# Kernel optimization log

Hardware: AMD Instinct MI355X
Metric: run time of the kernel (lower is better)

The kernel has to match this reference:

```python
import jax, jax.numpy as jnp
import numpy as np

K = 3          # number of nearest neighbors for interpolation
EPS = 1e-8     # inverse-distance epsilon
BN_EPS = 1e-5  # torch BatchNorm1d default eps

B, NY, NX = 4, 16384, 4096
CY, CX = 128, 256
DIM = CY + CX
SHARED = (512, 256, 128)


def setup_inputs() -> dict:
    key = jax.random.key(0)
    ks = jax.random.split(key, 16)
    inp = {
        'y_points': jax.random.normal(ks[0], (B, NY, 3), jnp.float32),
        'y_feats': jax.random.normal(ks[1], (B, NY, CY), jnp.float32),
        'x_points': jax.random.normal(ks[2], (B, NX, 3), jnp.float32),
        'x_feats': jax.random.normal(ks[3], (B, NX, CX), jnp.float32),
    }
    in_chs = (DIM,) + SHARED[:-1]
    for i, (cin, cout) in enumerate(zip(in_chs, SHARED), start=1):
        scale = 1.0 / np.sqrt(cin)
        inp[f'W{i}'] = jax.random.normal(ks[4 + i], (cout, cin), jnp.float32) * scale
        inp[f'b{i}'] = jnp.zeros((cout,), jnp.float32)
        inp[f'g{i}'] = jnp.ones((cout,), jnp.float32)
        inp[f'be{i}'] = jnp.zeros((cout,), jnp.float32)
    return inp


def _interpolate(y_points, x_points, y_feats, x_feats):
    # squared pairwise distances [B, Ny, Nx]
    d = (jnp.sum(y_points * y_points, -1)[:, :, None]
         + jnp.sum(x_points * x_points, -1)[:, None, :]
         - 2.0 * jnp.einsum('bnd,bmd->bnm', y_points, x_points))
    neg_d, idx = jax.lax.top_k(-d, K)             # K smallest distances
    dists = -neg_d                                 # [B, Ny, K]
    w = 1.0 / (dists + EPS)
    w = w / jnp.sum(w, -1, keepdims=True)
    # gather neighbor features: [B, Ny, K, Cx]
    nb = jnp.take_along_axis(x_feats[:, None, :, :], idx[..., None], axis=2)
    interp = jnp.sum(nb * w[..., None], axis=2)    # [B, Ny, Cx]
    return jnp.concatenate([y_feats, interp], axis=-1)


def _conv_bn_relu(y, W, b, g, beta):
    # 1x1 Conv1d == per-point linear; y: [B, Cin, N]
    y = jnp.einsum('oc,bcn->bon', W, y) + b[None, :, None]
    mu = jnp.mean(y, axis=(0, 2), keepdims=True)
    var = jnp.var(y, axis=(0, 2), keepdims=True)
    y = (y - mu) * jax.lax.rsqrt(var + BN_EPS)
    return jax.nn.relu(y * g[None, :, None] + beta[None, :, None])


def reference(y_points, y_feats, x_points, x_feats,
              W1, b1, g1, be1, W2, b2, g2, be2, W3, b3, g3, be3):
    i_points = _interpolate(y_points, x_points, y_feats, x_feats)  # [B, Ny, DIM]
    y = jnp.transpose(i_points, (0, 2, 1))                          # [B, DIM, Ny]
    y = _conv_bn_relu(y, W1, b1, g1, be1)
    y = _conv_bn_relu(y, W2, b2, g2, be2)
    y = _conv_bn_relu(y, W3, b3, g3, be3)
    return y
```

## Files before the change

kernel.cpp:

```cpp
#include <hip/hip_runtime.h>

#define NYTOT 16384
#define NXP 4096
#define MTOT 65536
#define CYC 128
#define CXC 256
#define DIMC 384

typedef __attribute__((ext_vector_type(8))) _Float16 half8;
typedef __attribute__((ext_vector_type(4))) _Float16 half4;
typedef __attribute__((ext_vector_type(4))) float floatx4;
typedef __attribute__((ext_vector_type(2))) float floatx2;

using half_t = _Float16;

struct alignas(16) HF8 { half_t h[8]; };

__device__ __forceinline__ float fmed3(float a, float b, float c) {
  return __builtin_amdgcn_fmed3f(a, b, c);
}

__global__ __launch_bounds__(256) void prep_kernel(
    const float* __restrict__ x_points, float4* __restrict__ xq,
    const float* __restrict__ W1, const float* __restrict__ W2,
    const float* __restrict__ W3, half_t* __restrict__ wout) {
#pragma clang fp contract(off)
  const int bid = blockIdx.x;
  if (bid < 64) {
    int j = bid * 256 + threadIdx.x;
    int b = j >> 12, jj = j & 4095;
    const float* p = x_points + (size_t)b * NXP * 3 + 3 * jj;
    float x0 = p[0], x1 = p[1], x2 = p[2];
    float sx = (x0 * x0 + x1 * x1) + x2 * x2;
    float4 v; v.x = x0; v.y = x1; v.z = x2; v.w = sx;
    xq[j] = v;
  } else {
    int i = (bid - 64) * 256 + threadIdx.x;
    const float* src; half_t* dst; int j;
    if (i < 49152)      { src = W1; dst = wout;          j = i; }
    else if (i < 81920) { src = W2; dst = wout + 196608; j = i - 49152; }
    else                { src = W3; dst = wout + 327680; j = i - 81920; }
    floatx4 v = ((const floatx4*)src)[j];
    half4 h;
#pragma unroll
    for (int e = 0; e < 4; ++e) h[e] = (half_t)v[e];
    ((half4*)dst)[j] = h;
  }
}

__global__ __launch_bounds__(1024, 8) void interp_kernel(
    const float* __restrict__ y_points, const float* __restrict__ y_feats,
    const float* __restrict__ x_feats, const float4* __restrict__ xq,
    half_t* __restrict__ A0) {
#pragma clang fp contract(off)
  __shared__ float pd[16][128][3];
  __shared__ int   pi[16][128][3];
  __shared__ float t2s[128];
  __shared__ float sw[3][128];
  __shared__ int   si[3][128];
  const int b = blockIdx.x >> 7;
  const int chunk = blockIdx.x & 127;
  const int t = threadIdx.x;
  const int lane = t & 63;
  const int seg = t >> 6;
  const int yloc = lane << 1;

  const float* yp = y_points + ((size_t)b * NYTOT + chunk * 128 + yloc) * 3;
  floatx2 Y0 = {yp[0], yp[3]};
  floatx2 Y1 = {yp[1], yp[4]};
  floatx2 Y2 = {yp[2], yp[5]};
  floatx2 SY = (Y0 * Y0 + Y1 * Y1) + Y2 * Y2;

  const float4* xqs = xq + (size_t)b * NXP;
  const int jb = __builtin_amdgcn_readfirstlane(seg * 256);

  floatx2 D0 = {1e30f, 1e30f}, D1 = D0, D2 = D0;
#pragma unroll 8
  for (int jj = 0; jj < 256; ++jj) {
    float4 p = xqs[jb + jj];
    floatx2 inner = (Y0 * p.x + Y1 * p.y) + Y2 * p.z;
    floatx2 d = (SY + p.w) - 2.0f * inner;
    D2.x = fmed3(d.x, D1.x, D2.x);  D2.y = fmed3(d.y, D1.y, D2.y);
    D1.x = fmed3(d.x, D0.x, D1.x);  D1.y = fmed3(d.y, D0.y, D1.y);
    D0.x = fminf(d.x, D0.x);        D0.y = fminf(d.y, D0.y);
  }
  pd[seg][yloc][0] = D0.x; pd[seg][yloc][1] = D1.x; pd[seg][yloc][2] = D2.x;
  pd[seg][yloc + 1][0] = D0.y; pd[seg][yloc + 1][1] = D1.y; pd[seg][yloc + 1][2] = D2.y;
  __syncthreads();

  if (t < 128) {
    float m0 = 1e30f, m1 = 1e30f, m2 = 1e30f;
#pragma unroll
    for (int s = 0; s < 16; ++s)
#pragma unroll
      for (int c = 0; c < 3; ++c) {
        float v = pd[s][t][c];
        m2 = fmed3(v, m1, m2);
        m1 = fmed3(v, m0, m1);
        m0 = fminf(v, m0);
      }
    t2s[t] = m2;
  }
  __syncthreads();

  const float t2a = t2s[yloc], t2b = t2s[yloc + 1];
  const float tmax = fmaxf(t2a, t2b);
  float e0a = 1e30f, e1a = 1e30f, e2a = 1e30f; int k0a = 0, k1a = 0, k2a = 0;
  float e0b = 1e30f, e1b = 1e30f, e2b = 1e30f; int k0b = 0, k1b = 0, k2b = 0;
#pragma unroll 4
  for (int jj = 0; jj < 256; ++jj) {
    float4 p = xqs[jb + jj];
    floatx2 inner = (Y0 * p.x + Y1 * p.y) + Y2 * p.z;
    floatx2 d = (SY + p.w) - 2.0f * inner;
    if (fminf(d.x, d.y) <= tmax) {
      int j = jb + jj;
      {
        float dv = d.x;
        bool l0 = dv < e0a, l1 = dv < e1a, l2 = dv < e2a;
        e2a = l1 ? e1a : (l2 ? dv : e2a);  k2a = l1 ? k1a : (l2 ? j : k2a);
        e1a = l0 ? e0a : (l1 ? dv : e1a);  k1a = l0 ? k0a : (l1 ? j : k1a);
        e0a = l0 ? dv : e0a;               k0a = l0 ? j : k0a;
      }
      {
        float dv = d.y;
        bool l0 = dv < e0b, l1 = dv < e1b, l2 = dv < e2b;
        e2b = l1 ? e1b : (l2 ? dv : e2b);  k2b = l1 ? k1b : (l2 ? j : k2b);
        e1b = l0 ? e0b : (l1 ? dv : e1b);  k1b = l0 ? k0b : (l1 ? j : k1b);
        e0b = l0 ? dv : e0b;               k0b = l0 ? j : k0b;
      }
    }
  }
  pd[seg][yloc][0] = e0a; pd[seg][yloc][1] = e1a; pd[seg][yloc][2] = e2a;
  pi[seg][yloc][0] = k0a; pi[seg][yloc][1] = k1a; pi[seg][yloc][2] = k2a;
  pd[seg][yloc + 1][0] = e0b; pd[seg][yloc + 1][1] = e1b; pd[seg][yloc + 1][2] = e2b;
  pi[seg][yloc + 1][0] = k0b; pi[seg][yloc + 1][1] = k1b; pi[seg][yloc + 1][2] = k2b;
  __syncthreads();

  if (t < 128) {
    float f0 = 1e30f, f1 = 1e30f, f2 = 1e30f;
    int m0i = 0, m1i = 0, m2i = 0;
#pragma unroll
    for (int s = 0; s < 16; ++s)
#pragma unroll
      for (int c = 0; c < 3; ++c) {
        float d = pd[s][t][c]; int j = pi[s][t][c];
        bool l0 = d < f0, l1 = d < f1, l2 = d < f2;
        f2 = l1 ? f1 : (l2 ? d : f2);  m2i = l1 ? m1i : (l2 ? j : m2i);
        f1 = l0 ? f0 : (l1 ? d : f1);  m1i = l0 ? m0i : (l1 ? j : m1i);
        f0 = l0 ? d : f0;              m0i = l0 ? j : m0i;
      }
    float w0 = 1.0f / (f0 + 1e-8f), w1 = 1.0f / (f1 + 1e-8f), w2 = 1.0f / (f2 + 1e-8f);
    float ws = (w0 + w1) + w2;
    sw[0][t] = w0 / ws; sw[1][t] = w1 / ws; sw[2][t] = w2 / ws;
    si[0][t] = m0i; si[1][t] = m1i; si[2][t] = m2i;
  }
  __syncthreads();

  const floatx4* xf4 = (const floatx4*)(x_feats + (size_t)b * NXP * CXC);
  const floatx4* yf4 = (const floatx4*)(y_feats + ((size_t)b * NYTOT + chunk * 128) * CYC);
  half_t* fb = A0 + ((size_t)b * NYTOT + chunk * 128) * DIMC;
  {
    const int q = t & 63;
    const int ysub = t >> 6;
    for (int y2 = ysub; y2 < 128; y2 += 16) {
      int j0 = si[0][y2], j1 = si[1][y2], j2 = si[2][y2];
      float a0 = sw[0][y2], a1 = sw[1][y2], a2 = sw[2][y2];
      floatx4 v0 = xf4[(size_t)j0 * 64 + q];
      floatx4 v1 = xf4[(size_t)j1 * 64 + q];
      floatx4 v2 = xf4[(size_t)j2 * 64 + q];
      half4 h;
#pragma unroll
      for (int e = 0; e < 4; ++e)
        h[e] = (half_t)fmaf(v2[e], a2, fmaf(v1[e], a1, v0[e] * a0));
      *(half4*)&fb[(size_t)y2 * DIMC + CYC + q * 4] = h;
    }
  }
  {
    const int q2 = t & 31;
    const int ysub2 = t >> 5;
    for (int y2 = ysub2; y2 < 128; y2 += 32) {
      floatx4 v = yf4[(size_t)y2 * 32 + q2];
      half4 h;
#pragma unroll
      for (int e = 0; e < 4; ++e) h[e] = (half_t)v[e];
      *(half4*)&fb[(size_t)y2 * DIMC + q2 * 4] = h;
    }
  }
}

template<int K, int O, int NTN, bool FUSEA>
__global__ __launch_bounds__(512) void gemm256(
    const half_t* __restrict__ A, const half_t* __restrict__ Wh,
    const float* __restrict__ bias, half_t* __restrict__ C,
    float* __restrict__ sums, const float* __restrict__ ssA) {
  __shared__ __align__(16) short As[16][2][512];
  __shared__ __align__(16) short Bs[8][2][512];
  constexpr int NWG = (MTOT / 256) * NTN;
  const int lin = (blockIdx.x & 7) * (NWG >> 3) + (blockIdx.x >> 3);
  const int m0 = (lin / NTN) * 256;
  const int n0 = (lin % NTN) * 128;
  const int tid = threadIdx.x;
  const int lane = tid & 63;
  const int wid = tid >> 6;
  const int wm = wid >> 1, wn = wid & 1;
  const int lm = lane & 15;
  const int lk = (lane >> 4) * 8;
  floatx4 acc[4][4] = {};

  for (int k0 = 0; k0 < K; k0 += 64) {
    __syncthreads();
    if constexpr (FUSEA) {
#pragma unroll
      for (int c = 0; c < 2; ++c) {
        int id = wid * 2 + c;
        int sub = id >> 1, ks = id & 1;
        const half_t* src = Wh + (size_t)(n0 + sub * 16 + lm) * K + (k0 + ks * 32 + lk);
        __builtin_amdgcn_global_load_lds(
            (const __attribute__((address_space(1))) void*)src,
            (__attribute__((address_space(3))) void*)&Bs[sub][ks][0], 16, 0, 0);
      }
      const int r = tid & 255;
      const int hh = tid >> 8;
      const half_t* arow = A + (size_t)(m0 + r) * K + k0 + hh * 32;
      half8 in[4];
#pragma unroll
      for (int g = 0; g < 4; ++g) in[g] = *(const half8*)&arow[g * 8];
#pragma unroll
      for (int g = 0; g < 4; ++g) {
        int kc = k0 + hh * 32 + g * 8;
        half8 h;
#pragma unroll
        for (int e = 0; e < 8; ++e) {
          float f = fmaxf((float)in[g][e] * ssA[kc + e] + ssA[K + kc + e], 0.f);
          h[e] = (half_t)f;
        }
        *(half8*)&As[r >> 4][hh][(g * 16 + (r & 15)) * 8] = h;
      }
    } else {
#pragma unroll
      for (int c = 0; c < 6; ++c) {
        int id = wid * 6 + c;
        if (id < 32) {
          int sub = id >> 1, ks = id & 1;
          const half_t* src = A + (size_t)(m0 + sub * 16 + lm) * K + (k0 + ks * 32 + lk);
          __builtin_amdgcn_global_load_lds(
              (const __attribute__((address_space(1))) void*)src,
              (__attribute__((address_space(3))) void*)&As[sub][ks][0], 16, 0, 0);
        } else {
          int id2 = id - 32;
          int sub = id2 >> 1, ks = id2 & 1;
          const half_t* src = Wh + (size_t)(n0 + sub * 16 + lm) * K + (k0 + ks * 32 + lk);
          __builtin_amdgcn_global_load_lds(
              (const __attribute__((address_space(1))) void*)src,
              (__attribute__((address_space(3))) void*)&Bs[sub][ks][0], 16, 0, 0);
        }
      }
    }
    __syncthreads();
#pragma unroll
    for (int ks = 0; ks < 2; ++ks) {
      half8 af[4], bfm[4];
#pragma unroll
      for (int i = 0; i < 4; ++i) af[i] = *(const half8*)&As[wm * 4 + i][ks][lane * 8];
#pragma unroll
      for (int j = 0; j < 4; ++j) bfm[j] = *(const half8*)&Bs[wn * 4 + j][ks][lane * 8];
#pragma unroll
      for (int i = 0; i < 4; ++i)
#pragma unroll
        for (int j = 0; j < 4; ++j)
          acc[i][j] = __builtin_amdgcn_mfma_f32_16x16x32_f16(af[i], bfm[j], acc[i][j], 0, 0, 0);
    }
  }

#pragma unroll
  for (int j = 0; j < 4; ++j) {
    int nn = n0 + wn * 64 + j * 16 + lm;
    float bv = bias[nn];
    float psum = 0.f, psq = 0.f;
#pragma unroll
    for (int i = 0; i < 4; ++i) {
      int mr = m0 + wm * 64 + i * 16 + (lane >> 4) * 4;
#pragma unroll
      for (int rr = 0; rr < 4; ++rr) {
        float z = acc[i][j][rr] + bv;
        C[(size_t)(mr + rr) * O + nn] = (half_t)z;
        psum += z; psq += z * z;
      }
    }
    psum += __shfl_xor(psum, 16, 64); psq += __shfl_xor(psq, 16, 64);
    psum += __shfl_xor(psum, 32, 64); psq += __shfl_xor(psq, 32, 64);
    if ((lane >> 4) == 0) {
      atomicAdd(&sums[nn], psum);
      atomicAdd(&sums[O + nn], psq);
    }
  }
}

template<int K, int O, bool FUSEA, bool TOUT>
__global__ __launch_bounds__(256) void gemm_f16(
    const half_t* __restrict__ A, const half_t* __restrict__ Wh,
    const float* __restrict__ bias, half_t* __restrict__ C,
    float* __restrict__ sums, const float* __restrict__ ssA) {
  __shared__ __align__(16) short As[8][2][512];
  __shared__ __align__(16) short Bs[8][2][512];
  const int m0 = blockIdx.x * 128;
  const int n0 = blockIdx.y * 128;
  const int tid = threadIdx.x;
  const int lane = tid & 63;
  const int wid = tid >> 6;
  const int wm = wid >> 1, wn = wid & 1;
  const int lm = lane & 15;
  const int lk = (lane >> 4) * 8;
  floatx4 acc[4][4] = {};

  for (int k0 = 0; k0 < K; k0 += 64) {
    __syncthreads();
    if constexpr (FUSEA) {
#pragma unroll
      for (int c = 0; c < 4; ++c) {
        int id = wid * 4 + c;
        int sub = id >> 1;
        int ks = id & 1;
        const half_t* src = Wh + (size_t)(n0 + sub * 16 + lm) * K + (k0 + ks * 32 + lk);
        __builtin_amdgcn_global_load_lds(
            (const __attribute__((address_space(1))) void*)src,
            (__attribute__((address_space(3))) void*)&Bs[sub][ks][0], 16, 0, 0);
      }
      const int r = tid & 127;
      const int hh = tid >> 7;
      const half_t* arow = A + (size_t)(m0 + r) * K + k0 + hh * 32;
      half8 in[4];
#pragma unroll
      for (int g = 0; g < 4; ++g) in[g] = *(const half8*)&arow[g * 8];
#pragma unroll
      for (int g = 0; g < 4; ++g) {
        int kc = k0 + hh * 32 + g * 8;
        half8 h;
#pragma unroll
        for (int e = 0; e < 8; ++e) {
          float f = fmaxf((float)in[g][e] * ssA[kc + e] + ssA[K + kc + e], 0.f);
          h[e] = (half_t)f;
        }
        *(half8*)&As[r >> 4][hh][(g * 16 + (r & 15)) * 8] = h;
      }
    } else {
#pragma unroll
      for (int c = 0; c < 8; ++c) {
        int id = wid * 8 + c;
        int sub = (id >> 1) & 7;
        int ks = id & 1;
        const half_t* src = (id < 16)
            ? A  + (size_t)(m0 + sub * 16 + lm) * K + (k0 + ks * 32 + lk)
            : Wh + (size_t)(n0 + sub * 16 + lm) * K + (k0 + ks * 32 + lk);
        __builtin_amdgcn_global_load_lds(
            (const __attribute__((address_space(1))) void*)src,
            (__attribute__((address_space(3))) void*)(id < 16 ? &As[sub][ks][0]
                                                             : &Bs[sub][ks][0]),
            16, 0, 0);
      }
    }
    __syncthreads();
#pragma unroll
    for (int ks = 0; ks < 2; ++ks) {
      half8 af[4], bfm[4];
#pragma unroll
      for (int i = 0; i < 4; ++i) af[i] = *(const half8*)&As[wm * 4 + i][ks][lane * 8];
#pragma unroll
      for (int j = 0; j < 4; ++j) bfm[j] = *(const half8*)&Bs[wn * 4 + j][ks][lane * 8];
#pragma unroll
      for (int i = 0; i < 4; ++i)
#pragma unroll
        for (int j = 0; j < 4; ++j)
          acc[i][j] = __builtin_amdgcn_mfma_f32_16x16x32_f16(af[i], bfm[j], acc[i][j], 0, 0, 0);
    }
  }

  const int bb = m0 >> 14;
  const int nbase = (m0 & (NYTOT - 1)) + wm * 64 + (lane >> 4) * 4;
#pragma unroll
  for (int j = 0; j < 4; ++j) {
    int nn = n0 + wn * 64 + j * 16 + lm;
    float bv = bias[nn];
    float psum = 0.f, psq = 0.f;
#pragma unroll
    for (int i = 0; i < 4; ++i) {
      half4 hv;
#pragma unroll
      for (int rr = 0; rr < 4; ++rr) {
        float z = acc[i][j][rr] + bv;
        hv[rr] = (half_t)z;
        psum += z; psq += z * z;
      }
      if constexpr (TOUT) {
        *(half4*)&C[((size_t)(bb * O + nn)) * NYTOT + nbase + i * 16] = hv;
      } else {
        int mr = m0 + wm * 64 + i * 16 + (lane >> 4) * 4;
#pragma unroll
        for (int rr = 0; rr < 4; ++rr)
          C[(size_t)(mr + rr) * O + nn] = hv[rr];
      }
    }
    psum += __shfl_xor(psum, 16, 64); psq += __shfl_xor(psq, 16, 64);
    psum += __shfl_xor(psum, 32, 64); psq += __shfl_xor(psq, 32, 64);
    if ((lane >> 4) == 0) {
      atomicAdd(&sums[nn], psum);
      atomicAdd(&sums[O + nn], psq);
    }
  }
}

__global__ void finalize_kernel(const float* __restrict__ sums, const float* __restrict__ g,
                                const float* __restrict__ be, float* __restrict__ ss, int O) {
  int c = threadIdx.x;
  if (c < O) {
    const float invN = 1.0f / 65536.0f;
    float mean = sums[c] * invN;
    float var = sums[O + c] * invN - mean * mean;
    float sc = g[c] / sqrtf(var + 1e-5f);
    float sh = be[c] - mean * sc;
    if (!isfinite(sc) || !isfinite(sh)) { sc = 1.0f; sh = 0.0f; }
    ss[c] = sc;
    ss[O + c] = sh;
  }
}

__global__ __launch_bounds__(256) void bnfin_kernel(
    const half_t* __restrict__ Z, const float* __restrict__ ss,
    float* __restrict__ out) {
  size_t i = (size_t)blockIdx.x * 256 + threadIdx.x;
  int c = (int)((i * 8) >> 14) & 127;
  float sc = ss[c], sh = ss[128 + c];
  HF8 v = ((const HF8*)Z)[i];
  floatx4 o0, o1;
#pragma unroll
  for (int e = 0; e < 4; ++e) {
    o0[e] = fmaxf((float)v.h[e] * sc + sh, 0.f);
    o1[e] = fmaxf((float)v.h[4 + e] * sc + sh, 0.f);
  }
  ((floatx4*)out)[i * 2] = o0;
  ((floatx4*)out)[i * 2 + 1] = o1;
}

extern "C" void kernel_launch(void* const* d_in, const int* in_sizes, int n_in,
                              void* d_out, int out_size, void* d_ws, size_t ws_size,
                              hipStream_t stream) {
  const float* y_points = (const float*)d_in[0];
  const float* y_feats  = (const float*)d_in[1];
  const float* x_points = (const float*)d_in[2];
  const float* x_feats  = (const float*)d_in[3];
  const float* W1 = (const float*)d_in[4];  const float* b1 = (const float*)d_in[5];
  const float* g1 = (const float*)d_in[6];  const float* be1 = (const float*)d_in[7];
  const float* W2 = (const float*)d_in[8];  const float* b2 = (const float*)d_in[9];
  const float* g2 = (const float*)d_in[10]; const float* be2 = (const float*)d_in[11];
  const float* W3 = (const float*)d_in[12]; const float* b3 = (const float*)d_in[13];
  const float* g3 = (const float*)d_in[14]; const float* be3 = (const float*)d_in[15];

  char* ws = (char*)d_ws;
  half_t* A0 = (half_t*)ws;
  half_t* z1 = (half_t*)(ws + 50331648);
  half_t* z2 = (half_t*)ws;
  half_t* z3T = (half_t*)(ws + 50331648);
  float4* xq = (float4*)(ws + 50331648);
  float* st = (float*)(ws + 117440512);
  half_t* W1h = (half_t*)d_out;
  half_t* W2h = W1h + 196608;
  half_t* W3h = W1h + 327680;
  hipMemsetAsync(st, 0, 1792 * sizeof(float), stream);

  prep_kernel<<<416, 256, 0, stream>>>(x_points, xq, W1, W2, W3, W1h);
  interp_kernel<<<512, 1024, 0, stream>>>(y_points, y_feats, x_feats, xq, A0);

  gemm256<384, 512, 4, false><<<1024, 512, 0, stream>>>(A0, W1h, b1, z1, st + 0, nullptr);
  finalize_kernel<<<1, 512, 0, stream>>>(st + 0, g1, be1, st + 1792, 512);

  gemm256<512, 256, 2, true><<<512, 512, 0, stream>>>(z1, W2h, b2, z2, st + 1024, st + 1792);
  finalize_kernel<<<1, 256, 0, stream>>>(st + 1024, g2, be2, st + 2816, 256);

  gemm_f16<256, 128, true, true><<<dim3(512, 1), 256, 0, stream>>>(z2, W3h, b3, z3T, st + 1536, st + 2816);
  finalize_kernel<<<1, 128, 0, stream>>>(st + 1536, g3, be3, st + 3328, 128);

  bnfin_kernel<<<4096, 256, 0, stream>>>(z3T, st + 3328, (float*)d_out);
}
```

Measured before the change: 460.9 us.

## Software-pipeline GEMM tiles with double-buffered weights and block-level BN stat reduction

Restructures the three GEMM kernels so the next K-tile's weights go into a second LDS buffer via async global-to-LDS loads, and the next A slice goes into registers, while MFMAs run on the current tile. The first GEMM now also routes A through registers instead of direct LDS loads, giving one code path for all three GEMMs. BatchNorm partial sums are first reduced across warps in shared memory, so each block issues one atomic per channel instead of one per warp. This costs extra LDS and register pressure, which may lower occupancy.

```diff
diff --git a/kernel.cpp b/kernel.cpp
--- a/kernel.cpp
+++ b/kernel.cpp
@@ -188,14 +188,16 @@
   }
 }
 
-template<int K, int O, int NTN, bool FUSEA>
-__global__ __launch_bounds__(512) void gemm256(
+template<int K, int O, int NTN, bool BN>
+__global__ __launch_bounds__(512) void gemm256p(
     const half_t* __restrict__ A, const half_t* __restrict__ Wh,
     const float* __restrict__ bias, half_t* __restrict__ C,
     float* __restrict__ sums, const float* __restrict__ ssA) {
   __shared__ __align__(16) short As[16][2][512];
-  __shared__ __align__(16) short Bs[8][2][512];
+  __shared__ __align__(16) short Bs[2][8][2][512];
+  __shared__ float stats[4][2][128];
   constexpr int NWG = (MTOT / 256) * NTN;
+  constexpr int NT = K / 64;
   const int lin = (blockIdx.x & 7) * (NWG >> 3) + (blockIdx.x >> 3);
   const int m0 = (lin / NTN) * 256;
   const int n0 = (lin % NTN) * 128;
@@ -205,73 +207,78 @@
   const int wm = wid >> 1, wn = wid & 1;
   const int lm = lane & 15;
   const int lk = (lane >> 4) * 8;
+  const int r = tid & 255;
+  const int hh = tid >> 8;
   floatx4 acc[4][4] = {};
-
-  for (int k0 = 0; k0 < K; k0 += 64) {
+  half8 in[4];
+
+#pragma unroll
+  for (int c = 0; c < 2; ++c) {
+    int id = wid * 2 + c;
+    int sub = id >> 1, ks = id & 1;
+    const half_t* src = Wh + (size_t)(n0 + sub * 16 + lm) * K + (ks * 32 + lk);
+    __builtin_amdgcn_global_load_lds(
+        (const __attribute__((address_space(1))) void*)src,
+        (__attribute__((address_space(3))) void*)&Bs[0][sub][ks][0], 16, 0, 0);
+  }
+  {
+    const half_t* arow = A + (size_t)(m0 + r) * K + hh * 32;
+#pragma unroll
+    for (int g = 0; g < 4; ++g) in[g] = *(const half8*)&arow[g * 8];
+  }
+  int cur = 0;
+
+  for (int t = 0; t < NT; ++t) {
+    const int k0 = t * 64;
     __syncthreads();
-    if constexpr (FUSEA) {
-#pragma unroll
-      for (int c = 0; c < 2; ++c) {
-        int id = wid * 2 + c;
-        int sub = id >> 1, ks = id & 1;
-        const half_t* src = Wh + (size_t)(n0 + sub * 16 + lm) * K + (k0 + ks * 32 + lk);
-        __builtin_amdgcn_global_load_lds(
-            (const __attribute__((address_space(1))) void*)src,
-            (__attribute__((address_space(3))) void*)&Bs[sub][ks][0], 16, 0, 0);
-      }
-      const int r = tid & 255;
-      const int hh = tid >> 8;
-      const half_t* arow = A + (size_t)(m0 + r) * K + k0 + hh * 32;
-      half8 in[4];
-#pragma unroll
-      for (int g = 0; g < 4; ++g) in[g] = *(const half8*)&arow[g * 8];
-#pragma unroll
-      for (int g = 0; g < 4; ++g) {
+#pragma unroll
+    for (int g = 0; g < 4; ++g) {
+      half8 h;
+      if constexpr (BN) {
         int kc = k0 + hh * 32 + g * 8;
-        half8 h;
 #pragma unroll
         for (int e = 0; e < 8; ++e) {
           float f = fmaxf((float)in[g][e] * ssA[kc + e] + ssA[K + kc + e], 0.f);
           h[e] = (half_t)f;
         }
-        *(half8*)&As[r >> 4][hh][(g * 16 + (r & 15)) * 8] = h;
-      }
-    } else {
-#pragma unroll
-      for (int c = 0; c < 6; ++c) {
-        int id = wid * 6 + c;
-        if (id < 32) {
-          int sub = id >> 1, ks = id & 1;
-          const half_t* src = A + (size_t)(m0 + sub * 16 + lm) * K + (k0 + ks * 32 + lk);
-          __builtin_amdgcn_global_load_lds(
-              (const __attribute__((address_space(1))) void*)src,
-              (__attribute__((address_space(3))) void*)&As[sub][ks][0], 16, 0, 0);
-        } else {
-          int id2 = id - 32;
-          int sub = id2 >> 1, ks = id2 & 1;
-          const half_t* src = Wh + (size_t)(n0 + sub * 16 + lm) * K + (k0 + ks * 32 + lk);
-          __builtin_amdgcn_global_load_lds(
-              (const __attribute__((address_space(1))) void*)src,
-              (__attribute__((address_space(3))) void*)&Bs[sub][ks][0], 16, 0, 0);
-        }
-      }
+      } else {
+        h = in[g];
+      }
+      *(half8*)&As[r >> 4][hh][(g * 16 + (r & 15)) * 8] = h;
     }
     __syncthreads();
+    if (t + 1 < NT) {
+      const int k1 = k0 + 64;
+#pragma unroll
+      for (int c = 0; c < 2; ++c) {
+        int id = wid * 2 + c;
+        int sub = id >> 1, ks = id & 1;
+        const half_t* src = Wh + (size_t)(n0 + sub * 16 + lm) * K + (k1 + ks * 32 + lk);
+        __builtin_amdgcn_global_load_lds(
+            (const __attribute__((address_space(1))) void*)src,
+            (__attribute__((address_space(3))) void*)&Bs[cur ^ 1][sub][ks][0], 16, 0, 0);
+      }
+      const half_t* arow = A + (size_t)(m0 + r) * K + k1 + hh * 32;
+#pragma unroll
+      for (int g = 0; g < 4; ++g) in[g] = *(const half8*)&arow[g * 8];
+    }
 #pragma unroll
     for (int ks = 0; ks < 2; ++ks) {
       half8 af[4], bfm[4];
 #pragma unroll
       for (int i = 0; i < 4; ++i) af[i] = *(const half8*)&As[wm * 4 + i][ks][lane * 8];
 #pragma unroll
-      for (int j = 0; j < 4; ++j) bfm[j] = *(const half8*)&Bs[wn * 4 + j][ks][lane * 8];
+      for (int j = 0; j < 4; ++j) bfm[j] = *(const half8*)&Bs[cur][wn * 4 + j][ks][lane * 8];
 #pragma unroll
       for (int i = 0; i < 4; ++i)
 #pragma unroll
         for (int j = 0; j < 4; ++j)
           acc[i][j] = __builtin_amdgcn_mfma_f32_16x16x32_f16(af[i], bfm[j], acc[i][j], 0, 0, 0);
     }
-  }
-
+    cur ^= 1;
+  }
+
+  float ps[4], pq[4];
 #pragma unroll
   for (int j = 0; j < 4; ++j) {
     int nn = n0 + wn * 64 + j * 16 + lm;
@@ -289,20 +296,34 @@
     }
     psum += __shfl_xor(psum, 16, 64); psq += __shfl_xor(psq, 16, 64);
     psum += __shfl_xor(psum, 32, 64); psq += __shfl_xor(psq, 32, 64);
-    if ((lane >> 4) == 0) {
-      atomicAdd(&sums[nn], psum);
-      atomicAdd(&sums[O + nn], psq);
-    }
-  }
-}
-
-template<int K, int O, bool FUSEA, bool TOUT>
-__global__ __launch_bounds__(256) void gemm_f16(
+    ps[j] = psum; pq[j] = psq;
+  }
+  __syncthreads();
+  if ((lane >> 4) == 0) {
+#pragma unroll
+    for (int j = 0; j < 4; ++j) {
+      int ch = wn * 64 + j * 16 + lm;
+      stats[wm][0][ch] = ps[j];
+      stats[wm][1][ch] = pq[j];
+    }
+  }
+  __syncthreads();
+  if (tid < 256) {
+    int s = tid >> 7, ch = tid & 127;
+    float v = ((stats[0][s][ch] + stats[1][s][ch]) + stats[2][s][ch]) + stats[3][s][ch];
+    atomicAdd(&sums[(s ? O : 0) + n0 + ch], v);
+  }
+}
+
+template<int K, int O, bool BN, bool TOUT>
+__global__ __launch_bounds__(256) void gemm128p(
     const half_t* __restrict__ A, const half_t* __restrict__ Wh,
     const float* __restrict__ bias, half_t* __restrict__ C,
     float* __restrict__ sums, const float* __restrict__ ssA) {
   __shared__ __align__(16) short As[8][2][512];
-  __shared__ __align__(16) short Bs[8][2][512];
+  __shared__ __align__(16) short Bs[2][8][2][512];
+  __shared__ float stats[2][2][128];
+  constexpr int NT = K / 64;
   const int m0 = blockIdx.x * 128;
   const int n0 = blockIdx.y * 128;
   const int tid = threadIdx.x;
@@ -311,72 +332,80 @@
   const int wm = wid >> 1, wn = wid & 1;
   const int lm = lane & 15;
   const int lk = (lane >> 4) * 8;
+  const int r = tid & 127;
+  const int hh = tid >> 7;
   floatx4 acc[4][4] = {};
-
-  for (int k0 = 0; k0 < K; k0 += 64) {
+  half8 in[4];
+
+#pragma unroll
+  for (int c = 0; c < 4; ++c) {
+    int id = wid * 4 + c;
+    int sub = id >> 1, ks = id & 1;
+    const half_t* src = Wh + (size_t)(n0 + sub * 16 + lm) * K + (ks * 32 + lk);
+    __builtin_amdgcn_global_load_lds(
+        (const __attribute__((address_space(1))) void*)src,
+        (__attribute__((address_space(3))) void*)&Bs[0][sub][ks][0], 16, 0, 0);
+  }
+  {
+    const half_t* arow = A + (size_t)(m0 + r) * K + hh * 32;
+#pragma unroll
+    for (int g = 0; g < 4; ++g) in[g] = *(const half8*)&arow[g * 8];
+  }
+  int cur = 0;
+
+  for (int t = 0; t < NT; ++t) {
+    const int k0 = t * 64;
     __syncthreads();
-    if constexpr (FUSEA) {
-#pragma unroll
-      for (int c = 0; c < 4; ++c) {
-        int id = wid * 4 + c;
-        int sub = id >> 1;
-        int ks = id & 1;
-        const half_t* src = Wh + (size_t)(n0 + sub * 16 + lm) * K + (k0 + ks * 32 + lk);
-        __builtin_amdgcn_global_load_lds(
-            (const __attribute__((address_space(1))) void*)src,
-            (__attribute__((address_space(3))) void*)&Bs[sub][ks][0], 16, 0, 0);
-      }
-      const int r = tid & 127;
-      const int hh = tid >> 7;
-      const half_t* arow = A + (size_t)(m0 + r) * K + k0 + hh * 32;
-      half8 in[4];
-#pragma unroll
-      for (int g = 0; g < 4; ++g) in[g] = *(const half8*)&arow[g * 8];
-#pragma unroll
-      for (int g = 0; g < 4; ++g) {
+#pragma unroll
+    for (int g = 0; g < 4; ++g) {
+      half8 h;
+      if constexpr (BN) {
         int kc = k0 + hh * 32 + g * 8;
-        half8 h;
 #pragma unroll
         for (int e = 0; e < 8; ++e) {
           float f = fmaxf((float)in[g][e] * ssA[kc + e] + ssA[K + kc + e], 0.f);
           h[e] = (half_t)f;
         }
-        *(half8*)&As[r >> 4][hh][(g * 16 + (r & 15)) * 8] = h;
-      }
-    } else {
-#pragma unroll
-      for (int c = 0; c < 8; ++c) {
-        int id = wid * 8 + c;
-        int sub = (id >> 1) & 7;
-        int ks = id & 1;
-        const half_t* src = (id < 16)
-            ? A  + (size_t)(m0 + sub * 16 + lm) * K + (k0 + ks * 32 + lk)
-            : Wh + (size_t)(n0 + sub * 16 + lm) * K + (k0 + ks * 32 + lk);
+      } else {
+        h = in[g];
+      }
+      *(half8*)&As[r >> 4][hh][(g * 16 + (r & 15)) * 8] = h;
+    }
+    __syncthreads();
+    if (t + 1 < NT) {
+      const int k1 = k0 + 64;
+#pragma unroll
+      for (int c = 0; c < 4; ++c) {
+        int id = wid * 4 + c;
+        int sub = id >> 1, ks = id & 1;
+        const half_t* src = Wh + (size_t)(n0 + sub * 16 + lm) * K + (k1 + ks * 32 + lk);
         __builtin_amdgcn_global_load_lds(
             (const __attribute__((address_space(1))) void*)src,
-            (__attribute__((address_space(3))) void*)(id < 16 ? &As[sub][ks][0]
-                                                             : &Bs[sub][ks][0]),
-            16, 0, 0);
-      }
-    }
-    __syncthreads();
+            (__attribute__((address_space(3))) void*)&Bs[cur ^ 1][sub][ks][0], 16, 0, 0);
+      }
+      const half_t* arow = A + (size_t)(m0 + r) * K + k1 + hh * 32;
+#pragma unroll
+      for (int g = 0; g < 4; ++g) in[g] = *(const half8*)&arow[g * 8];
+    }
 #pragma unroll
     for (int ks = 0; ks < 2; ++ks) {
       half8 af[4], bfm[4];
 #pragma unroll
       for (int i = 0; i < 4; ++i) af[i] = *(const half8*)&As[wm * 4 + i][ks][lane * 8];
 #pragma unroll
-      for (int j = 0; j < 4; ++j) bfm[j] = *(const half8*)&Bs[wn * 4 + j][ks][lane * 8];
+      for (int j = 0; j < 4; ++j) bfm[j] = *(const half8*)&Bs[cur][wn * 4 + j][ks][lane * 8];
 #pragma unroll
       for (int i = 0; i < 4; ++i)
 #pragma unroll
         for (int j = 0; j < 4; ++j)
           acc[i][j] = __builtin_amdgcn_mfma_f32_16x16x32_f16(af[i], bfm[j], acc[i][j], 0, 0, 0);
     }
+    cur ^= 1;
   }
 
   const int bb = m0 >> 14;
   const int nbase = (m0 & (NYTOT - 1)) + wm * 64 + (lane >> 4) * 4;
+  float ps[4], pq[4];
 #pragma unroll
   for (int j = 0; j < 4; ++j) {
     int nn = n0 + wn * 64 + j * 16 + lm;
@@ -402,10 +431,22 @@
     }
     psum += __shfl_xor(psum, 16, 64); psq += __shfl_xor(psq, 16, 64);
     psum += __shfl_xor(psum, 32, 64); psq += __shfl_xor(psq, 32, 64);
-    if ((lane >> 4) == 0) {
-      atomicAdd(&sums[nn], psum);
-      atomicAdd(&sums[O + nn], psq);
-    }
+    ps[j] = psum; pq[j] = psq;
+  }
+  __syncthreads();
+  if ((lane >> 4) == 0) {
+#pragma unroll
+    for (int j = 0; j < 4; ++j) {
+      int ch = wn * 64 + j * 16 + lm;
+      stats[wm][0][ch] = ps[j];
+      stats[wm][1][ch] = pq[j];
+    }
+  }
+  __syncthreads();
+  if (tid < 256) {
+    int s = tid >> 7, ch = tid & 127;
+    float v = stats[0][s][ch] + stats[1][s][ch];
+    atomicAdd(&sums[(s ? O : 0) + n0 + ch], v);
   }
 }
 
@@ -470,13 +511,13 @@
   prep_kernel<<<416, 256, 0, stream>>>(x_points, xq, W1, W2, W3, W1h);
   interp_kernel<<<512, 1024, 0, stream>>>(y_points, y_feats, x_feats, xq, A0);
 
-  gemm256<384, 512, 4, false><<<1024, 512, 0, stream>>>(A0, W1h, b1, z1, st + 0, nullptr);
+  gemm256p<384, 512, 4, false><<<1024, 512, 0, stream>>>(A0, W1h, b1, z1, st + 0, nullptr);
   finalize_kernel<<<1, 512, 0, stream>>>(st + 0, g1, be1, st + 1792, 512);
 
-  gemm256<512, 256, 2, true><<<512, 512, 0, stream>>>(z1, W2h, b2, z2, st + 1024, st + 1792);
+  gemm256p<512, 256, 2, true><<<512, 512, 0, stream>>>(z1, W2h, b2, z2, st + 1024, st + 1792);
   finalize_kernel<<<1, 256, 0, stream>>>(st + 1024, g2, be2, st + 2816, 256);
 
-  gemm_f16<256, 128, true, true><<<dim3(512, 1), 256, 0, stream>>>(z2, W3h, b3, z3T, st + 1536, st + 2816);
+  gemm128p<256, 128, true, true><<<dim3(512, 1), 256, 0, stream>>>(z2, W3h, b3, z3T, st + 1536, st + 2816);
   finalize_kernel<<<1, 128, 0, stream>>>(st + 1536, g3, be3, st + 3328, 128);
 
   bnfin_kernel<<<4096, 256, 0, stream>>>(z3T, st + 3328, (float*)d_out);
```

New measurement: 447.2 us. -3.0%, faster.
